# Kernel optimization log

Measured on AMD Instinct MI355X. Metric: run time of the kernel, lower is better.

The kernel has to match this reference:

```python
import jax, jax.numpy as jnp
import numpy as np

BS, QLEN, DIM, NH = 4, 2048, 1024, 16
DH = DIM // NH
NEG = float(np.finfo(np.float32).min)


def setup_inputs() -> dict:
    key = jax.random.key(0)
    ks = jax.random.split(key, 10)
    s = 1.0 / np.sqrt(DIM)
    return {
        "hidden_states": jax.random.normal(ks[0], (BS, QLEN, DIM), jnp.float32),
        "attention_mask": jnp.ones((BS, QLEN), jnp.int32),
        "Wq": jax.random.normal(ks[1], (DIM, DIM), jnp.float32) * s,
        "bq": jnp.zeros((DIM,), jnp.float32),
        "Wk": jax.random.normal(ks[2], (DIM, DIM), jnp.float32) * s,
        "bk": jnp.zeros((DIM,), jnp.float32),
        "Wv": jax.random.normal(ks[3], (DIM, DIM), jnp.float32) * s,
        "bv": jnp.zeros((DIM,), jnp.float32),
        "Wo": jax.random.normal(ks[4], (DIM, DIM), jnp.float32) * s,
        "bo": jnp.zeros((DIM,), jnp.float32),
    }


def _heads(x, bs):
    # [bs, len, dim] -> [bs, n_heads, len, dim_per_head]
    return x.reshape(bs, -1, NH, DH).transpose(0, 2, 1, 3)


def reference(hidden_states, attention_mask, Wq, bq, Wk, bk, Wv, bv, Wo, bo):
    bs, qlen, dim = hidden_states.shape
    q = _heads(hidden_states @ Wq.T + bq, bs) / jnp.sqrt(jnp.asarray(DH, hidden_states.dtype))
    k = _heads(hidden_states @ Wk.T + bk, bs)
    v = _heads(hidden_states @ Wv.T + bv, bs)
    scores = jnp.einsum("bhqd,bhkd->bhqk", q, k)  # [bs, nh, qlen, klen]
    mask = (attention_mask == 0)[:, None, None, :]  # [bs,1,1,klen]
    scores = jnp.where(mask, NEG, scores)
    weights = jax.nn.softmax(scores.astype(jnp.float32), axis=-1).astype(scores.dtype)
    context = jnp.einsum("bhqk,bhkd->bhqd", weights, v)
    context = context.transpose(0, 2, 1, 3).reshape(bs, qlen, dim)
    return context @ Wo.T + bo
```

## Files before the change

### kernel.cpp

```cpp
#include <hip/hip_runtime.h>
#include <hip/hip_bf16.h>

#define BS 4
#define QLEN 2048
#define DIM 1024
#define NH 16
#define DH 64

typedef __attribute__((ext_vector_type(8))) short bf16x8;
typedef __attribute__((ext_vector_type(4))) float f32x4;
typedef __attribute__((ext_vector_type(16))) float f32x16;
typedef __attribute__((ext_vector_type(2))) unsigned int u32x2;
typedef __attribute__((ext_vector_type(4))) unsigned int u32x4;
typedef unsigned short u16;
typedef unsigned int u32;
typedef unsigned long long u64;

#define LOG2E 1.44269504088896f

__device__ __forceinline__ u32 cvtpk_bf16(float lo, float hi) {
    u32 r;
    asm("v_cvt_pk_bf16_f32 %0, %1, %2" : "=v"(r) : "v"(lo), "v"(hi));
    return r;
}
__device__ __forceinline__ u16 f2bf_hw(float f) { return (u16)cvtpk_bf16(f, f); }

__device__ __forceinline__ void async_lds16(const void* gp, void* lp) {
    __builtin_amdgcn_global_load_lds(
        (const __attribute__((address_space(1))) u32*)(u64)gp,
        (__attribute__((address_space(3))) u32*)(u32)(u64)lp,
        16, 0, 0);
}

__global__ void cvt_fused(const float* __restrict__ H,
                          const float* __restrict__ W0, const float* __restrict__ W1,
                          const float* __restrict__ W2, const float* __restrict__ W3,
                          u16* __restrict__ Hb,
                          u16* __restrict__ D0, u16* __restrict__ D1,
                          u16* __restrict__ D2, u16* __restrict__ D3) {
    const int h4 = (BS * QLEN * DIM) / 4;
    int i = blockIdx.x * blockDim.x + threadIdx.x;
    const float* s;
    u16* d;
    int off;
    if (i < h4) { s = H; d = Hb; off = i; }
    else {
        int j = i - h4;
        int ws = j >> 18;
        off = j & 262143;
        s = ws == 0 ? W0 : ws == 1 ? W1 : ws == 2 ? W2 : W3;
        d = ws == 0 ? D0 : ws == 1 ? D1 : ws == 2 ? D2 : D3;
    }
    float4 v = ((const float4*)s)[off];
    uint2 o;
    o.x = cvtpk_bf16(v.x, v.y);
    o.y = cvtpk_bf16(v.z, v.w);
    ((uint2*)d)[off] = o;
}

__global__ void mask_prep(const int* __restrict__ mask, float* __restrict__ maskF,
                          int* __restrict__ flags) {
    const int tile = blockIdx.x;
    const int lane = threadIdx.x;
    const int idx = tile * 64 + lane;
    const int v = mask[idx];
    maskF[idx] = v ? 1.0f : 0.0f;
    u64 bal = __ballot(v == 0);
    if (lane == 0) flags[tile] = (bal != 0ull) ? 1 : 0;
}

__global__ __launch_bounds__(256) void gemm_qkv(
    const u16* __restrict__ Hb,
    const u16* __restrict__ Wq, const u16* __restrict__ Wk, const u16* __restrict__ Wv,
    const float* __restrict__ bq, const float* __restrict__ bk, const float* __restrict__ bvv,
    u16* __restrict__ Qb, u16* __restrict__ Kb, u16* __restrict__ Vt)
{
    __shared__ __align__(16) u16 As[128 * 32];
    __shared__ __align__(16) u16 Bs[128 * 32];
    const int z = blockIdx.z;
    const u16* W = z == 0 ? Wq : z == 1 ? Wk : Wv;
    const float* bias = z == 0 ? bq : z == 1 ? bk : bvv;
    const int t = threadIdx.x;
    const int w = t >> 6, lane = t & 63;
    const int lr = lane & 15, lg = lane >> 4;
    const int m0 = blockIdx.y * 128, n0 = blockIdx.x * 128;
    const int wm = (w >> 1) * 64, wn = (w & 1) * 64;
    const int srow = w * 16 + (lane >> 2);
    const int sk = (lane & 3) * 8;

    f32x4 acc[4][4] = {};

    for (int kt = 0; kt < DIM; kt += 32) {
        __syncthreads();
        async_lds16(Hb + (u64)(m0 + srow) * DIM + kt + sk,      &As[(w * 16) * 32]);
        async_lds16(Hb + (u64)(m0 + 64 + srow) * DIM + kt + sk, &As[(64 + w * 16) * 32]);
        async_lds16(W + (u64)(n0 + srow) * DIM + kt + sk,       &Bs[(w * 16) * 32]);
        async_lds16(W + (u64)(n0 + 64 + srow) * DIM + kt + sk,  &Bs[(64 + w * 16) * 32]);
        __syncthreads();
        bf16x8 a[4], b[4];
#pragma unroll
        for (int i = 0; i < 4; ++i) a[i] = *(const bf16x8*)&As[(wm + i * 16 + lr) * 32 + lg * 8];
#pragma unroll
        for (int i = 0; i < 4; ++i) b[i] = *(const bf16x8*)&Bs[(wn + i * 16 + lr) * 32 + lg * 8];
#pragma unroll
        for (int mi = 0; mi < 4; ++mi)
#pragma unroll
            for (int ni = 0; ni < 4; ++ni)
                acc[mi][ni] = __builtin_amdgcn_mfma_f32_16x16x32_bf16(a[mi], b[ni], acc[mi][ni], 0, 0, 0);
    }

#pragma unroll
    for (int mi = 0; mi < 4; ++mi)
#pragma unroll
        for (int ni = 0; ni < 4; ++ni) {
            const int col = n0 + wn + ni * 16 + lr;
            const float bb = bias[col];
#pragma unroll
            for (int r = 0; r < 4; ++r) {
                const int row = m0 + wm + mi * 16 + lg * 4 + r;
                const float v = acc[mi][ni][r] + bb;
                const int bh = (row >> 11) * NH + (col >> 6);
                const int q = row & (QLEN - 1);
                const int d = col & (DH - 1);
                if (z == 0)      Qb[((u64)bh * QLEN + q) * DH + d] = f2bf_hw(v * (0.125f * LOG2E));
                else if (z == 1) Kb[((u64)bh * QLEN + q) * DH + d] = f2bf_hw(v);
                else             Vt[((u64)bh * DH + d) * QLEN + q] = f2bf_hw(v);
            }
        }
}

__global__ __launch_bounds__(256) void gemm_o(
    const u16* __restrict__ A, const u16* __restrict__ W,
    const float* __restrict__ bias, float* __restrict__ ofp)
{
    __shared__ __align__(16) u16 As[128 * 32];
    __shared__ __align__(16) u16 Bs[128 * 32];
    const int t = threadIdx.x;
    const int w = t >> 6, lane = t & 63;
    const int lr = lane & 15, lg = lane >> 4;
    const int m0 = blockIdx.y * 128, n0 = blockIdx.x * 128;
    const int wm = (w >> 1) * 64, wn = (w & 1) * 64;
    const int srow = w * 16 + (lane >> 2);
    const int sk = (lane & 3) * 8;

    f32x4 acc[4][4] = {};

    for (int kt = 0; kt < DIM; kt += 32) {
        __syncthreads();
        async_lds16(A + (u64)(m0 + srow) * DIM + kt + sk,      &As[(w * 16) * 32]);
        async_lds16(A + (u64)(m0 + 64 + srow) * DIM + kt + sk, &As[(64 + w * 16) * 32]);
        async_lds16(W + (u64)(n0 + srow) * DIM + kt + sk,      &Bs[(w * 16) * 32]);
        async_lds16(W + (u64)(n0 + 64 + srow) * DIM + kt + sk, &Bs[(64 + w * 16) * 32]);
        __syncthreads();
        bf16x8 a[4], b[4];
#pragma unroll
        for (int i = 0; i < 4; ++i) a[i] = *(const bf16x8*)&As[(wm + i * 16 + lr) * 32 + lg * 8];
#pragma unroll
        for (int i = 0; i < 4; ++i) b[i] = *(const bf16x8*)&Bs[(wn + i * 16 + lr) * 32 + lg * 8];
#pragma unroll
        for (int mi = 0; mi < 4; ++mi)
#pragma unroll
            for (int ni = 0; ni < 4; ++ni)
                acc[mi][ni] = __builtin_amdgcn_mfma_f32_16x16x32_bf16(a[mi], b[ni], acc[mi][ni], 0, 0, 0);
    }

#pragma unroll
    for (int mi = 0; mi < 4; ++mi)
#pragma unroll
        for (int ni = 0; ni < 4; ++ni) {
            const int col = n0 + wn + ni * 16 + lr;
            const float bb = bias[col];
#pragma unroll
            for (int r = 0; r < 4; ++r) {
                const int row = m0 + wm + mi * 16 + lg * 4 + r;
                ofp[(u64)row * DIM + col] = acc[mi][ni][r] + bb;
            }
        }
}

__global__ __launch_bounds__(256) void attn_kernel(
    const u16* __restrict__ Qb, const u16* __restrict__ Kb, const u16* __restrict__ Vt,
    const float* __restrict__ maskF, const int* __restrict__ mflags, u16* __restrict__ ctx)
{
    __shared__ __align__(16) u16 Ks[2][64 * 64];
    __shared__ __align__(16) u16 Vs[2][64 * 64];

    const int t = threadIdx.x;
    const int w = t >> 6, lane = t & 63;
    const int l5 = lane & 31, hi = lane >> 5, l7 = lane & 7;

    const int id = blockIdx.x + 16 * blockIdx.y;
    const int v = (id & 7) * 128 + (id >> 3);
    const int qt = v & 15, bh = v >> 4;
    const int b = bh >> 4, hh = bh & 15;
    const int q0 = qt * 128;

    const u16* Kbh = Kb + (u64)bh * QLEN * DH;
    const u16* Vth = Vt + (u64)bh * DH * QLEN;
    const float* mFb = maskF + b * QLEN;
    const int* flb = mflags + b * (QLEN / 64);

    const u64 fmask = __ballot(flb[lane & 31] != 0);

    const u16* qp = Qb + ((u64)bh * QLEN + q0 + w * 32 + l5) * DH + hi * 8;
    bf16x8 bq[4];
#pragma unroll
    for (int dc = 0; dc < 4; ++dc) bq[dc] = *(const bf16x8*)(qp + dc * 16);

    f32x16 o[2] = {};
    float mrun = -3.0e38f, lsum = 0.f;

    const int srow = lane >> 3, schunk = lane & 7;

#define STAGE(BUF, KT) do {                                                            \
    _Pragma("unroll")                                                                  \
    for (int c = 0; c < 2; ++c) {                                                      \
        const int row_ = w * 16 + c * 8 + srow;                                        \
        const int ch_ = schunk ^ (row_ & 7);                                           \
        async_lds16(Kbh + (u64)((KT) + row_) * DH + ch_ * 8, &Ks[BUF][(w * 16 + c * 8) * 64]); \
        async_lds16(Vth + (u64)row_ * QLEN + (KT) + ch_ * 8, &Vs[BUF][(w * 16 + c * 8) * 64]); \
    } } while (0)

    STAGE(0, 0);
    __syncthreads();

    int buf = 0;
    for (int kt = 0; kt < QLEN; kt += 64) {
        if (kt + 64 < QLEN) STAGE(buf ^ 1, kt + 64);

        const char* Kbase = (const char*)&Ks[buf][0];
        const char* Vbase = (const char*)&Vs[buf][0];

        f32x16 s[2] = {};
        __builtin_amdgcn_s_setprio(1);
#pragma unroll
        for (int dc = 0; dc < 4; ++dc) {
            const u32 off = (u32)(l5 * 128) + (u32)(((2 * dc + hi) ^ l7) << 4);
            bf16x8 ak0 = *(const bf16x8*)(Kbase + off);
            bf16x8 ak1 = *(const bf16x8*)(Kbase + off + 4096);
            s[0] = __builtin_amdgcn_mfma_f32_32x32x16_bf16(ak0, bq[dc], s[0], 0, 0, 0);
            s[1] = __builtin_amdgcn_mfma_f32_32x32x16_bf16(ak1, bq[dc], s[1], 0, 0, 0);
        }
        __builtin_amdgcn_s_setprio(0);

        float mx[16];
#pragma unroll
        for (int i = 0; i < 16; ++i) mx[i] = fmaxf(s[0][i], s[1][i]);
#pragma unroll
        for (int st = 8; st > 0; st >>= 1)
#pragma unroll
            for (int i = 0; i < 16; ++i) if (i < st) mx[i] = fmaxf(mx[i], mx[i + st]);
        const float tma = fmaxf(mx[0], __shfl_xor(mx[0], 32));

        if (!__all(tma <= mrun + 11.5415603f)) {
            const float nm = fmaxf(mrun, tma);
            const float corr = exp2f(mrun - nm);
            mrun = nm;
            lsum *= corr;
#pragma unroll
            for (int i = 0; i < 16; ++i) { o[0][i] *= corr; o[1][i] *= corr; }
        }

#pragma unroll
        for (int i = 0; i < 16; ++i) {
            s[0][i] = exp2f(s[0][i] - mrun);
            s[1][i] = exp2f(s[1][i] - mrun);
        }

        if ((fmask >> (kt >> 6)) & 1ull) {
#pragma unroll
            for (int kb = 0; kb < 2; ++kb)
#pragma unroll
                for (int m = 0; m < 4; ++m) {
                    float4 mm = *(const float4*)&mFb[kt + kb * 32 + m * 8 + hi * 4];
                    s[kb][4 * m + 0] *= mm.x;
                    s[kb][4 * m + 1] *= mm.y;
                    s[kb][4 * m + 2] *= mm.z;
                    s[kb][4 * m + 3] *= mm.w;
                }
        }

        {
            float ps[16];
#pragma unroll
            for (int i = 0; i < 16; ++i) ps[i] = s[0][i] + s[1][i];
#pragma unroll
            for (int st = 8; st > 0; st >>= 1)
#pragma unroll
                for (int i = 0; i < 16; ++i) if (i < st) ps[i] += ps[i + st];
            lsum += ps[0];
        }

        __builtin_amdgcn_s_setprio(1);
#pragma unroll
        for (int kc = 0; kc < 4; ++kc) {
            const int kb = kc >> 1;
            const int base = 8 * (kc & 1);
            const u32 P00 = cvtpk_bf16(s[kb][base + 0], s[kb][base + 1]);
            const u32 P01 = cvtpk_bf16(s[kb][base + 2], s[kb][base + 3]);
            const u32 P10 = cvtpk_bf16(s[kb][base + 4], s[kb][base + 5]);
            const u32 P11 = cvtpk_bf16(s[kb][base + 6], s[kb][base + 7]);
            u32x2 w02 = __builtin_amdgcn_permlane32_swap(P00, P10, false, false);
            u32x2 w13 = __builtin_amdgcn_permlane32_swap(P01, P11, false, false);
            u32x4 words;
            words.x = w02[0]; words.y = w13[0]; words.z = w02[1]; words.w = w13[1];
            const bf16x8 bp = __builtin_bit_cast(bf16x8, words);

            const u32 voff = (u32)(l5 * 128) + (u32)(((2 * kc + hi) ^ l7) << 4);
            bf16x8 av0 = *(const bf16x8*)(Vbase + voff);
            bf16x8 av1 = *(const bf16x8*)(Vbase + voff + 4096);
            o[0] = __builtin_amdgcn_mfma_f32_32x32x16_bf16(av0, bp, o[0], 0, 0, 0);
            o[1] = __builtin_amdgcn_mfma_f32_32x32x16_bf16(av1, bp, o[1], 0, 0, 0);
        }
        __builtin_amdgcn_s_setprio(0);

        __syncthreads();
        buf ^= 1;
    }
#undef STAGE

    const float lall = lsum + __shfl_xor(lsum, 32);
    const float inv = 1.0f / fmaxf(lall, 1e-37f);

    u16* cp = ctx + (((u64)b * QLEN + (q0 + w * 32 + l5)) * NH + hh) * DH;
#pragma unroll
    for (int db = 0; db < 2; ++db)
#pragma unroll
        for (int m = 0; m < 4; ++m) {
            const int d0 = db * 32 + m * 8 + hi * 4;
            const u32 wA = cvtpk_bf16(o[db][4 * m + 0] * inv, o[db][4 * m + 1] * inv);
            const u32 wB = cvtpk_bf16(o[db][4 * m + 2] * inv, o[db][4 * m + 3] * inv);
            *(u32*)(cp + d0) = wA;
            *(u32*)(cp + d0 + 2) = wB;
        }
}

extern "C" void kernel_launch(void* const* d_in, const int* in_sizes, int n_in,
                              void* d_out, int out_size, void* d_ws, size_t ws_size,
                              hipStream_t stream) {
    const float* H    = (const float*)d_in[0];
    const int*   mask = (const int*)d_in[1];
    const float* Wq   = (const float*)d_in[2];
    const float* bq   = (const float*)d_in[3];
    const float* Wk   = (const float*)d_in[4];
    const float* bk   = (const float*)d_in[5];
    const float* Wv   = (const float*)d_in[6];
    const float* bv   = (const float*)d_in[7];
    const float* Wo   = (const float*)d_in[8];
    const float* bo   = (const float*)d_in[9];
    float* out = (float*)d_out;

    const u64 NTOK = (u64)BS * QLEN;
    const u64 HN = NTOK * DIM;
    const u64 WN = (u64)DIM * DIM;

    u16* Hb  = (u16*)d_ws;
    u16* Wqb = Hb + HN;
    u16* Wkb = Wqb + WN;
    u16* Wvb = Wkb + WN;
    u16* Wob = Wvb + WN;
    u16* Qb  = Wob + WN;
    u16* Kb  = Qb + HN;
    u16* Vtg = Kb + HN;
    u16* Ctx = Vtg + HN;
    float* maskF = (float*)(Ctx + HN);
    int* mflags = (int*)(maskF + BS * QLEN);

    cvt_fused<<<12288, 256, 0, stream>>>(H, Wq, Wk, Wv, Wo, Hb, Wqb, Wkb, Wvb, Wob);
    mask_prep<<<BS * (QLEN / 64), 64, 0, stream>>>(mask, maskF, mflags);

    gemm_qkv<<<dim3(DIM / 128, (int)(NTOK / 128), 3), 256, 0, stream>>>(
        Hb, Wqb, Wkb, Wvb, bq, bk, bv, Qb, Kb, Vtg);

    attn_kernel<<<dim3(QLEN / 128, BS * NH), 256, 0, stream>>>(Qb, Kb, Vtg, maskF, mflags, Ctx);

    gemm_o<<<dim3(DIM / 128, (int)(NTOK / 128)), 256, 0, stream>>>(Ctx, Wob, bo, out);
}
```

Before: 270.8 us.

## Enlarge attention blocks to 256 queries with 4-stage K/V LDS ring pipeline

The attention kernel now uses 512-thread blocks covering 256 queries each, so every K/V tile staged in LDS is shared by twice as many waves. Staging moves from a double buffer with a full __syncthreads per tile to a four-slot ring with two tiles in flight, gated by explicit vmcnt waits and s_barrier. V fragments are read from LDS before the softmax so those reads overlap the exp work. This aims to cut global K/V traffic and barrier stalls, at the cost of more LDS per block, higher register pressure, and fewer independent blocks.

```diff
diff --git a/kernel.cpp b/kernel.cpp
--- a/kernel.cpp
+++ b/kernel.cpp
@@ -178,22 +178,22 @@
         }
 }
 
-__global__ __launch_bounds__(256) void attn_kernel(
+__global__ __launch_bounds__(512) void attn_kernel(
     const u16* __restrict__ Qb, const u16* __restrict__ Kb, const u16* __restrict__ Vt,
     const float* __restrict__ maskF, const int* __restrict__ mflags, u16* __restrict__ ctx)
 {
-    __shared__ __align__(16) u16 Ks[2][64 * 64];
-    __shared__ __align__(16) u16 Vs[2][64 * 64];
+    __shared__ __align__(16) u16 Ks[4][64 * 64];
+    __shared__ __align__(16) u16 Vs[4][64 * 64];
 
     const int t = threadIdx.x;
     const int w = t >> 6, lane = t & 63;
     const int l5 = lane & 31, hi = lane >> 5, l7 = lane & 7;
 
-    const int id = blockIdx.x + 16 * blockIdx.y;
-    const int v = (id & 7) * 128 + (id >> 3);
-    const int qt = v & 15, bh = v >> 4;
+    const int id = blockIdx.x + 8 * blockIdx.y;
+    const int v = (id & 7) * 64 + (id >> 3);
+    const int qt = v & 7, bh = v >> 3;
     const int b = bh >> 4, hh = bh & 15;
-    const int q0 = qt * 128;
+    const int q0 = qt * 256;
 
     const u16* Kbh = Kb + (u64)bh * QLEN * DH;
     const u16* Vth = Vt + (u64)bh * DH * QLEN;
@@ -210,26 +210,17 @@
     f32x16 o[2] = {};
     float mrun = -3.0e38f, lsum = 0.f;
 
-    const int srow = lane >> 3, schunk = lane & 7;
-
-#define STAGE(BUF, KT) do {                                                            \
-    _Pragma("unroll")                                                                  \
-    for (int c = 0; c < 2; ++c) {                                                      \
-        const int row_ = w * 16 + c * 8 + srow;                                        \
-        const int ch_ = schunk ^ (row_ & 7);                                           \
-        async_lds16(Kbh + (u64)((KT) + row_) * DH + ch_ * 8, &Ks[BUF][(w * 16 + c * 8) * 64]); \
-        async_lds16(Vth + (u64)row_ * QLEN + (KT) + ch_ * 8, &Vs[BUF][(w * 16 + c * 8) * 64]); \
-    } } while (0)
-
-    STAGE(0, 0);
-    __syncthreads();
-
-    int buf = 0;
-    for (int kt = 0; kt < QLEN; kt += 64) {
-        if (kt + 64 < QLEN) STAGE(buf ^ 1, kt + 64);
-
-        const char* Kbase = (const char*)&Ks[buf][0];
-        const char* Vbase = (const char*)&Vs[buf][0];
+    const int srow = w * 8 + (lane >> 3);
+    const int sch = l7 ^ (srow & 7);
+
+    auto STAGE = [&](int B, int KT) {
+        async_lds16(Kbh + (u64)(KT * 64 + srow) * DH + sch * 8, &Ks[B][(w * 8) * 64]);
+        async_lds16(Vth + (u64)srow * QLEN + KT * 64 + sch * 8, &Vs[B][(w * 8) * 64]);
+    };
+
+    auto compute = [&](int B, int kt64) {
+        const char* Kbase = (const char*)&Ks[B][0];
+        const char* Vbase = (const char*)&Vs[B][0];
 
         f32x16 s[2] = {};
         __builtin_amdgcn_s_setprio(1);
@@ -243,6 +234,14 @@
         }
         __builtin_amdgcn_s_setprio(0);
 
+        bf16x8 av0[4], av1[4];
+#pragma unroll
+        for (int kc = 0; kc < 4; ++kc) {
+            const u32 voff = (u32)(l5 * 128) + (u32)(((2 * kc + hi) ^ l7) << 4);
+            av0[kc] = *(const bf16x8*)(Vbase + voff);
+            av1[kc] = *(const bf16x8*)(Vbase + voff + 4096);
+        }
+
         float mx[16];
 #pragma unroll
         for (int i = 0; i < 16; ++i) mx[i] = fmaxf(s[0][i], s[1][i]);
@@ -267,12 +266,12 @@
             s[1][i] = exp2f(s[1][i] - mrun);
         }
 
-        if ((fmask >> (kt >> 6)) & 1ull) {
+        if ((fmask >> kt64) & 1ull) {
 #pragma unroll
             for (int kb = 0; kb < 2; ++kb)
 #pragma unroll
                 for (int m = 0; m < 4; ++m) {
-                    float4 mm = *(const float4*)&mFb[kt + kb * 32 + m * 8 + hi * 4];
+                    float4 mm = *(const float4*)&mFb[kt64 * 64 + kb * 32 + m * 8 + hi * 4];
                     s[kb][4 * m + 0] *= mm.x;
                     s[kb][4 * m + 1] *= mm.y;
                     s[kb][4 * m + 2] *= mm.z;
@@ -306,18 +305,29 @@
             words.x = w02[0]; words.y = w13[0]; words.z = w02[1]; words.w = w13[1];
             const bf16x8 bp = __builtin_bit_cast(bf16x8, words);
 
-            const u32 voff = (u32)(l5 * 128) + (u32)(((2 * kc + hi) ^ l7) << 4);
-            bf16x8 av0 = *(const bf16x8*)(Vbase + voff);
-            bf16x8 av1 = *(const bf16x8*)(Vbase + voff + 4096);
-            o[0] = __builtin_amdgcn_mfma_f32_32x32x16_bf16(av0, bp, o[0], 0, 0, 0);
-            o[1] = __builtin_amdgcn_mfma_f32_32x32x16_bf16(av1, bp, o[1], 0, 0, 0);
+            o[0] = __builtin_amdgcn_mfma_f32_32x32x16_bf16(av0[kc], bp, o[0], 0, 0, 0);
+            o[1] = __builtin_amdgcn_mfma_f32_32x32x16_bf16(av1[kc], bp, o[1], 0, 0, 0);
         }
         __builtin_amdgcn_s_setprio(0);
-
-        __syncthreads();
-        buf ^= 1;
+    };
+
+    STAGE(0, 0);
+    STAGE(1, 1);
+    for (int tt = 0; tt < 30; ++tt) {
+        STAGE((tt + 2) & 3, tt + 2);
+        asm volatile("s_waitcnt vmcnt(4)" ::: "memory");
+        __builtin_amdgcn_s_barrier();
+        __builtin_amdgcn_sched_barrier(0);
+        compute(tt & 3, tt);
     }
-#undef STAGE
+    asm volatile("s_waitcnt vmcnt(2)" ::: "memory");
+    __builtin_amdgcn_s_barrier();
+    __builtin_amdgcn_sched_barrier(0);
+    compute(30 & 3, 30);
+    asm volatile("s_waitcnt vmcnt(0)" ::: "memory");
+    __builtin_amdgcn_s_barrier();
+    __builtin_amdgcn_sched_barrier(0);
+    compute(31 & 3, 31);
 
     const float lall = lsum + __shfl_xor(lsum, 32);
     const float inv = 1.0f / fmaxf(lall, 1e-37f);
@@ -372,7 +382,7 @@
     gemm_qkv<<<dim3(DIM / 128, (int)(NTOK / 128), 3), 256, 0, stream>>>(
         Hb, Wqb, Wkb, Wvb, bq, bk, bv, Qb, Kb, Vtg);
 
-    attn_kernel<<<dim3(QLEN / 128, BS * NH), 256, 0, stream>>>(Qb, Kb, Vtg, maskF, mflags, Ctx);
+    attn_kernel<<<dim3(QLEN / 256, BS * NH), 512, 0, stream>>>(Qb, Kb, Vtg, maskF, mflags, Ctx);
 
     gemm_o<<<dim3(DIM / 128, (int)(NTOK / 128)), 256, 0, stream>>>(Ctx, Wob, bo, out);
 }
```

Measured after the change: 251.1 us. 1.08x faster.
